# Optimization experiments

Hardware: AMD Instinct MI355X
Metric: run time of the kernel (lower is better)

The kernel has to match this reference:

```python
import jax, jax.numpy as jnp
import numpy as np
from jax import lax

BN_EPS = 1e-3  # keras BatchNormalization default epsilon
DN = ('NHWC', 'HWIO', 'NHWC')


def ste_sign(x):
    # larq ste_sign forward: sign with sign(0) -> +1
    return jnp.where(x >= 0, 1.0, -1.0).astype(x.dtype)


def bn_inference(x, beta, mean, var):
    # scale=False -> no gamma, center=True -> beta
    return (x - mean) * lax.rsqrt(var + BN_EPS) + beta


def setup_inputs() -> dict:
    key = jax.random.key(0)
    ks = jax.random.split(key, 8)
    C = 256
    x = jax.random.normal(ks[0], (32, 56, 56, C), dtype=jnp.float32)
    w1 = jax.random.normal(ks[1], (3, 3, C, C), dtype=jnp.float32) * 0.05
    w2 = jax.random.normal(ks[2], (3, 3, C, C), dtype=jnp.float32) * 0.05
    beta1 = jax.random.normal(ks[3], (C,), dtype=jnp.float32) * 0.1
    beta2 = jax.random.normal(ks[4], (C,), dtype=jnp.float32) * 0.1
    mean1 = jax.random.normal(ks[5], (C,), dtype=jnp.float32) * 0.1
    mean2 = jax.random.normal(ks[6], (C,), dtype=jnp.float32) * 0.1
    var1 = jax.random.uniform(ks[7], (C,), dtype=jnp.float32, minval=0.5, maxval=1.5)
    var2 = jax.random.uniform(jax.random.fold_in(key, 7), (C,), dtype=jnp.float32, minval=0.5, maxval=1.5)
    return {"x": x, "w1": w1, "beta1": beta1, "mean1": mean1, "var1": var1,
            "w2": w2, "beta2": beta2, "mean2": mean2, "var2": var2}


def reference(x, w1, beta1, mean1, var1, w2, beta2, mean2, var2):
    # conv_1: quantized input and quantized weights (XNOR conv), stride 1, SAME
    h = lax.conv_general_dilated(ste_sign(x), ste_sign(w1), (1, 1), 'SAME',
                                 dimension_numbers=DN)
    h = bn_inference(h, beta1, mean1, var1)
    # conv_2: quantized input and weights
    h = lax.conv_general_dilated(ste_sign(h), ste_sign(w2), (1, 1), 'SAME',
                                 dimension_numbers=DN)
    # max pool 2x2 stride 2
    h = lax.reduce_window(h, -jnp.inf, lax.max, (1, 2, 2, 1), (1, 2, 2, 1), 'VALID')
    h = bn_inference(h, beta2, mean2, var2)
    return h
```

## Files before the change

kernel.cpp:

```cpp
#include <hip/hip_runtime.h>
#include <stdint.h>

#define BN_EPS 1e-3f

constexpr int Bn = 32, H = 56, Wd = 56, C = 256;
constexpr int NSLOT = 232;
typedef int v4i __attribute__((ext_vector_type(4)));

__device__ __forceinline__ int imax(int a, int b) { return a > b ? a : b; }

__global__ __launch_bounds__(256) void k_sign_x(const float* __restrict__ x,
                                                int8_t* __restrict__ xs, int n4) {
  int i = blockIdx.x * 256 + threadIdx.x;
  if (i >= n4) return;
  float4 v = ((const float4*)x)[i];
  char4 s;
  s.x = v.x >= 0.f ? 1 : -1;
  s.y = v.y >= 0.f ? 1 : -1;
  s.z = v.z >= 0.f ? 1 : -1;
  s.w = v.w >= 0.f ? 1 : -1;
  ((char4*)xs)[i] = s;
}

__global__ __launch_bounds__(256) void k_sign_wT2(const float* __restrict__ w,
                                                  uint32_t* __restrict__ wt) {
  int u = blockIdx.x * 256 + threadIdx.x;
  int f = u >> 8, r = u & 255;
  int l = r >> 2, w4 = r & 3;
  int grp = l >> 4, lid = l & 15;
  int tap = f >> 6, icq = (f >> 4) & 3, ocg = f & 15;
  int oc = ocg * 16 + lid;
  uint32_t pk = 0;
#pragma unroll
  for (int j = 0; j < 4; ++j) {
    int ic = icq * 64 + grp * 16 + w4 * 4 + j;
    float v = w[((size_t)(tap * 256 + ic)) * 256 + oc];
    pk |= (v >= 0.f ? 0x01u : 0xFFu) << (8 * j);
  }
  wt[u] = pk;
}

template <int MODE, int MS, int MSB>
__device__ __forceinline__ void conv_body(
    const int8_t* As, const int8_t* __restrict__ wT2, int wn, int lane,
    const float* __restrict__ beta, const float* __restrict__ mean,
    const float* __restrict__ var, int8_t* __restrict__ hs,
    float* __restrict__ outp, int b, int rp)
{
  const int grp = lane >> 4, lid = lane & 15;
  const int wbase = wn * 64;
  const int cstg = grp << 4;

  int sb[MS];
#pragma unroll
  for (int ms = 0; ms < MS; ++ms) {
    const int m = (MSB + ms) * 16 + lid;
    sb[ms] = (m & 1) * 58 + (m >> 1);
  }

  const int8_t* bpl = wT2 + (size_t)wn * 4096 + (size_t)lane * 16;

  v4i acc[MS][4];
#pragma unroll
  for (int i = 0; i < MS; ++i)
#pragma unroll
    for (int j = 0; j < 4; ++j) acc[i][j] = (v4i){0, 0, 0, 0};

#define LOADB(dst, st)                                                     \
  {                                                                        \
    const int8_t* p_ = bpl + (size_t)(st) * 16384;                         \
    _Pragma("unroll") for (int ns = 0; ns < 4; ++ns)                       \
        dst[ns] = *(const v4i*)(p_ + ns * 1024);                           \
  }

#define LOADA(dst, st)                                                     \
  {                                                                        \
    const int tap_ = (st) >> 2, icq_ = (st) & 3;                           \
    const int ky_ = (tap_ >= 6) ? 2 : ((tap_ >= 3) ? 1 : 0);               \
    const int kx_ = tap_ - 3 * ky_;                                        \
    const int D_ = ky_ * 58 + kx_;                                         \
    const int ko_ = cstg + icq_ * 64;                                      \
    _Pragma("unroll") for (int ms = 0; ms < MS; ++ms) {                    \
      const int s_ = sb[ms] + D_;                                          \
      dst[ms] = *(const v4i*)(As + (s_ << 8) + (ko_ ^ ((s_ & 7) << 4)));   \
    }                                                                      \
  }

#define MFMAC(af, bf)                                                      \
  __builtin_amdgcn_s_setprio(1);                                           \
  _Pragma("unroll") for (int ms = 0; ms < MS; ++ms)                        \
  _Pragma("unroll") for (int ns = 0; ns < 4; ++ns)                         \
      acc[ms][ns] = __builtin_amdgcn_mfma_i32_16x16x64_i8(                 \
          af[ms], bf[ns], acc[ms][ns], 0, 0, 0);                           \
  __builtin_amdgcn_s_setprio(0);

  v4i af[MS], bfA[4], bfB[4];
  LOADB(bfA, 0)

#pragma unroll 1
  for (int i = 0; i < 18; ++i) {
    const int s0 = 2 * i, s1 = 2 * i + 1;
    const int s2 = (s1 + 1 > 35) ? 35 : s1 + 1;
    LOADB(bfB, s1)
    LOADA(af, s0)
    __builtin_amdgcn_sched_barrier(0);
    MFMAC(af, bfA)
    LOADB(bfA, s2)
    LOADA(af, s1)
    __builtin_amdgcn_sched_barrier(0);
    MFMAC(af, bfB)
  }

#undef MFMAC
#undef LOADA
#undef LOADB

  const int rA = rp * 2;
  if (MODE == 0) {
#pragma unroll
    for (int ns = 0; ns < 4; ++ns) {
      const int oc = wbase + ns * 16 + lid;
      const float mu = mean[oc], rs = rsqrtf(var[oc] + BN_EPS), be = beta[oc];
#pragma unroll
      for (int ms = 0; ms < MS; ++ms)
#pragma unroll
        for (int q = 0; q < 4; ++q) {
          const int m = (MSB + ms) * 16 + grp * 4 + q;
          const int lr = m & 1, col = m >> 1;
          const float bnv = ((float)acc[ms][ns][q] - mu) * rs + be;
          hs[(((size_t)(b * 56 + rA + lr)) * 56 + col) * 256 + oc] =
              bnv >= 0.f ? (int8_t)1 : (int8_t)-1;
        }
    }
  } else {
#pragma unroll
    for (int ns = 0; ns < 4; ++ns) {
      const int oc = wbase + ns * 16 + lid;
      const float mu = mean[oc], rs = rsqrtf(var[oc] + BN_EPS), be = beta[oc];
#pragma unroll
      for (int ms = 0; ms < MS; ++ms) {
        const int mx = imax(imax(acc[ms][ns][0], acc[ms][ns][1]),
                            imax(acc[ms][ns][2], acc[ms][ns][3]));
        const int j = (MSB + ms) * 4 + grp;
        outp[(((size_t)(b * 28 + rp)) * 28 + j) * 256 + oc] =
            ((float)mx - mu) * rs + be;
      }
    }
  }
}

template <int MODE>
__global__ __launch_bounds__(512, 4) void k_conv(
    const int8_t* __restrict__ src, const int8_t* __restrict__ wT2,
    const float* __restrict__ beta, const float* __restrict__ mean,
    const float* __restrict__ var,
    int8_t* __restrict__ hs, float* __restrict__ outp)
{
  const int t = threadIdx.x;
  const int rp = blockIdx.x;
  const int b = blockIdx.y;
  const int rr0 = rp * 2;

  __shared__ __align__(16) int8_t As[NSLOT * 256];

  for (int i = t; i < NSLOT * 16; i += 512) {
    const int s = i >> 4, c = i & 15;
    const int lr = s / 58, colst = s - lr * 58;
    const int sr = rr0 + lr - 1, sc = colst - 1;
    uint4 v;
    v.x = v.y = v.z = v.w = 0u;
    if ((unsigned)sr < 56u && (unsigned)sc < 56u)
      v = *(const uint4*)(src + (((size_t)(b * 56 + sr)) * 56 + sc) * 256 + c * 16);
    *(uint4*)(As + (s << 8) + ((c << 4) ^ ((s & 7) << 4))) = v;
  }
  __syncthreads();

  const int lane = t & 63;
  const int wv = t >> 6;
  const int wm = wv >> 2, wn = wv & 3;
  if (wm == 0)
    conv_body<MODE, 4, 0>(As, wT2, wn, lane, beta, mean, var, hs, outp, b, rp);
  else
    conv_body<MODE, 3, 4>(As, wT2, wn, lane, beta, mean, var, hs, outp, b, rp);
}

extern "C" void kernel_launch(void* const* d_in, const int* in_sizes, int n_in,
                              void* d_out, int out_size, void* d_ws, size_t ws_size,
                              hipStream_t stream) {
  const float* x     = (const float*)d_in[0];
  const float* w1    = (const float*)d_in[1];
  const float* beta1 = (const float*)d_in[2];
  const float* mean1 = (const float*)d_in[3];
  const float* var1  = (const float*)d_in[4];
  const float* w2    = (const float*)d_in[5];
  const float* beta2 = (const float*)d_in[6];
  const float* mean2 = (const float*)d_in[7];
  const float* var2  = (const float*)d_in[8];
  float* out = (float*)d_out;

  const size_t NPIX = (size_t)Bn * H * Wd * C;
  int8_t* xs  = (int8_t*)d_ws;
  int8_t* hs  = xs + NPIX;
  int8_t* w1t = hs + NPIX;
  int8_t* w2t = w1t + 589824;

  k_sign_x<<<dim3((int)(NPIX / 4 / 256)), 256, 0, stream>>>(x, xs, (int)(NPIX / 4));
  k_sign_wT2<<<dim3(576), 256, 0, stream>>>(w1, (uint32_t*)w1t);
  k_sign_wT2<<<dim3(576), 256, 0, stream>>>(w2, (uint32_t*)w2t);
  k_conv<0><<<dim3(28, Bn), 512, 0, stream>>>(xs, w1t, beta1, mean1, var1, hs, nullptr);
  k_conv<1><<<dim3(28, Bn), 512, 0, stream>>>(hs, w2t, beta2, mean2, var2, nullptr, out);
}
```

Before: 137.9 us.

## Fuse input sign quantization into conv1 staging and hand-pipeline weight loads

Removes the separate sign kernel for x: the first conv block now reads fp32 input and packs signs into int8 while filling shared memory. This avoids the extra launch and the int8 intermediate write/read. It adds redundant fp32 reads of halo rows across blocks. Weight fragment loads are now issued via inline asm with explicit vmcnt waits to overlap global loads with MFMA work.

```diff
diff --git a/kernel.cpp b/kernel.cpp
--- a/kernel.cpp
+++ b/kernel.cpp
@@ -9,17 +9,10 @@
 
 __device__ __forceinline__ int imax(int a, int b) { return a > b ? a : b; }
 
-__global__ __launch_bounds__(256) void k_sign_x(const float* __restrict__ x,
-                                                int8_t* __restrict__ xs, int n4) {
-  int i = blockIdx.x * 256 + threadIdx.x;
-  if (i >= n4) return;
-  float4 v = ((const float4*)x)[i];
-  char4 s;
-  s.x = v.x >= 0.f ? 1 : -1;
-  s.y = v.y >= 0.f ? 1 : -1;
-  s.z = v.z >= 0.f ? 1 : -1;
-  s.w = v.w >= 0.f ? 1 : -1;
-  ((char4*)xs)[i] = s;
+__device__ __forceinline__ uint32_t pack4(float4 f) {
+  return (f.x >= 0.f ? 0x01u : 0xFFu) | ((f.y >= 0.f ? 0x01u : 0xFFu) << 8) |
+         ((f.z >= 0.f ? 0x01u : 0xFFu) << 16) |
+         ((f.w >= 0.f ? 0x01u : 0xFFu) << 24);
 }
 
 __global__ __launch_bounds__(256) void k_sign_wT2(const float* __restrict__ w,
@@ -39,6 +32,43 @@
   }
   wt[u] = pk;
 }
+
+#define ISSUEB(dst, st)                                                     \
+  {                                                                         \
+    const uint64_t a_ = bbase + (uint64_t)(uint32_t)(st) * 16384u;          \
+    asm volatile(                                                           \
+        "global_load_dwordx4 %0, %4, off\n\t"                               \
+        "global_load_dwordx4 %1, %4, off offset:1024\n\t"                   \
+        "global_load_dwordx4 %2, %4, off offset:2048\n\t"                   \
+        "global_load_dwordx4 %3, %4, off offset:3072"                       \
+        : "=&v"(dst[0]), "=&v"(dst[1]), "=&v"(dst[2]), "=&v"(dst[3])        \
+        : "v"(a_));                                                         \
+  }
+
+#define WAITVM(n)                                                           \
+  asm volatile("s_waitcnt vmcnt(" #n ")" ::: "memory");                     \
+  __builtin_amdgcn_sched_barrier(0);
+
+#define LOADA(dst, st)                                                      \
+  {                                                                         \
+    const int tap_ = (st) >> 2, icq_ = (st) & 3;                            \
+    const int ky_ = (tap_ >= 6) ? 2 : ((tap_ >= 3) ? 1 : 0);                \
+    const int kx_ = tap_ - 3 * ky_;                                         \
+    const int D_ = ky_ * 58 + kx_;                                          \
+    const int ko_ = cstg + icq_ * 64;                                       \
+    _Pragma("unroll") for (int ms = 0; ms < MS; ++ms) {                     \
+      const int s_ = sb[ms] + D_;                                           \
+      dst[ms] = *(const v4i*)(As + (s_ << 8) + (ko_ ^ ((s_ & 7) << 4)));    \
+    }                                                                       \
+  }
+
+#define MFMAC(af, bf)                                                       \
+  __builtin_amdgcn_s_setprio(1);                                            \
+  _Pragma("unroll") for (int ms = 0; ms < MS; ++ms)                         \
+  _Pragma("unroll") for (int ns = 0; ns < 4; ++ns)                          \
+      acc[ms][ns] = __builtin_amdgcn_mfma_i32_16x16x64_i8(                  \
+          af[ms], bf[ns], acc[ms][ns], 0, 0, 0);                            \
+  __builtin_amdgcn_s_setprio(0);
 
 template <int MODE, int MS, int MSB>
 __device__ __forceinline__ void conv_body(
@@ -58,7 +88,8 @@
     sb[ms] = (m & 1) * 58 + (m >> 1);
   }
 
-  const int8_t* bpl = wT2 + (size_t)wn * 4096 + (size_t)lane * 16;
+  const uint64_t bbase =
+      (uint64_t)(uintptr_t)(wT2 + (size_t)wn * 4096 + (size_t)lane * 16);
 
   v4i acc[MS][4];
 #pragma unroll
@@ -66,54 +97,28 @@
 #pragma unroll
     for (int j = 0; j < 4; ++j) acc[i][j] = (v4i){0, 0, 0, 0};
 
-#define LOADB(dst, st)                                                     \
-  {                                                                        \
-    const int8_t* p_ = bpl + (size_t)(st) * 16384;                         \
-    _Pragma("unroll") for (int ns = 0; ns < 4; ++ns)                       \
-        dst[ns] = *(const v4i*)(p_ + ns * 1024);                           \
-  }
-
-#define LOADA(dst, st)                                                     \
-  {                                                                        \
-    const int tap_ = (st) >> 2, icq_ = (st) & 3;                           \
-    const int ky_ = (tap_ >= 6) ? 2 : ((tap_ >= 3) ? 1 : 0);               \
-    const int kx_ = tap_ - 3 * ky_;                                        \
-    const int D_ = ky_ * 58 + kx_;                                         \
-    const int ko_ = cstg + icq_ * 64;                                      \
-    _Pragma("unroll") for (int ms = 0; ms < MS; ++ms) {                    \
-      const int s_ = sb[ms] + D_;                                          \
-      dst[ms] = *(const v4i*)(As + (s_ << 8) + (ko_ ^ ((s_ & 7) << 4)));   \
-    }                                                                      \
-  }
-
-#define MFMAC(af, bf)                                                      \
-  __builtin_amdgcn_s_setprio(1);                                           \
-  _Pragma("unroll") for (int ms = 0; ms < MS; ++ms)                        \
-  _Pragma("unroll") for (int ns = 0; ns < 4; ++ns)                         \
-      acc[ms][ns] = __builtin_amdgcn_mfma_i32_16x16x64_i8(                 \
-          af[ms], bf[ns], acc[ms][ns], 0, 0, 0);                           \
-  __builtin_amdgcn_s_setprio(0);
-
-  v4i af[MS], bfA[4], bfB[4];
-  LOADB(bfA, 0)
+  v4i af[MS], bf0[4], bf1[4];
+  ISSUEB(bf0, 0)
 
 #pragma unroll 1
-  for (int i = 0; i < 18; ++i) {
-    const int s0 = 2 * i, s1 = 2 * i + 1;
-    const int s2 = (s1 + 1 > 35) ? 35 : s1 + 1;
-    LOADB(bfB, s1)
+  for (int i = 0; i < 17; ++i) {
+    const int s0 = 2 * i, s1 = s0 + 1;
+    ISSUEB(bf1, s1)
     LOADA(af, s0)
-    __builtin_amdgcn_sched_barrier(0);
-    MFMAC(af, bfA)
-    LOADB(bfA, s2)
+    WAITVM(4)
+    MFMAC(af, bf0)
+    ISSUEB(bf0, s0 + 2)
     LOADA(af, s1)
-    __builtin_amdgcn_sched_barrier(0);
-    MFMAC(af, bfB)
-  }
-
-#undef MFMAC
-#undef LOADA
-#undef LOADB
+    WAITVM(4)
+    MFMAC(af, bf1)
+  }
+  ISSUEB(bf1, 35)
+  LOADA(af, 34)
+  WAITVM(4)
+  MFMAC(af, bf0)
+  LOADA(af, 35)
+  WAITVM(0)
+  MFMAC(af, bf1)
 
   const int rA = rp * 2;
   if (MODE == 0) {
@@ -151,7 +156,7 @@
 
 template <int MODE>
 __global__ __launch_bounds__(512, 4) void k_conv(
-    const int8_t* __restrict__ src, const int8_t* __restrict__ wT2,
+    const void* __restrict__ srcv, const int8_t* __restrict__ wT2,
     const float* __restrict__ beta, const float* __restrict__ mean,
     const float* __restrict__ var,
     int8_t* __restrict__ hs, float* __restrict__ outp)
@@ -169,8 +174,18 @@
     const int sr = rr0 + lr - 1, sc = colst - 1;
     uint4 v;
     v.x = v.y = v.z = v.w = 0u;
-    if ((unsigned)sr < 56u && (unsigned)sc < 56u)
-      v = *(const uint4*)(src + (((size_t)(b * 56 + sr)) * 56 + sc) * 256 + c * 16);
+    if ((unsigned)sr < 56u && (unsigned)sc < 56u) {
+      if (MODE == 0) {
+        const float* p = (const float*)srcv +
+                         ((((size_t)(b * 56 + sr)) * 56 + sc) * 256 + c * 16);
+        const float4* p4 = (const float4*)p;
+        v.x = pack4(p4[0]); v.y = pack4(p4[1]);
+        v.z = pack4(p4[2]); v.w = pack4(p4[3]);
+      } else {
+        v = *(const uint4*)((const int8_t*)srcv +
+                            (((size_t)(b * 56 + sr)) * 56 + sc) * 256 + c * 16);
+      }
+    }
     *(uint4*)(As + (s << 8) + ((c << 4) ^ ((s & 7) << 4))) = v;
   }
   __syncthreads();
@@ -199,14 +214,12 @@
   float* out = (float*)d_out;
 
   const size_t NPIX = (size_t)Bn * H * Wd * C;
-  int8_t* xs  = (int8_t*)d_ws;
-  int8_t* hs  = xs + NPIX;
+  int8_t* hs  = (int8_t*)d_ws;
   int8_t* w1t = hs + NPIX;
   int8_t* w2t = w1t + 589824;
 
-  k_sign_x<<<dim3((int)(NPIX / 4 / 256)), 256, 0, stream>>>(x, xs, (int)(NPIX / 4));
   k_sign_wT2<<<dim3(576), 256, 0, stream>>>(w1, (uint32_t*)w1t);
   k_sign_wT2<<<dim3(576), 256, 0, stream>>>(w2, (uint32_t*)w2t);
-  k_conv<0><<<dim3(28, Bn), 512, 0, stream>>>(xs, w1t, beta1, mean1, var1, hs, nullptr);
+  k_conv<0><<<dim3(28, Bn), 512, 0, stream>>>(x, w1t, beta1, mean1, var1, hs, nullptr);
   k_conv<1><<<dim3(28, Bn), 512, 0, stream>>>(hs, w2t, beta2, mean2, var2, nullptr, out);
 }
```

Result: slower. 148.9 us (+8.0%).
